# Kernel tuning notes

Hardware: AMD Instinct MI355X
Metric: run time of the kernel (lower is better)

## Reference

```python
import jax, jax.numpy as jnp
import numpy as np
import math

EMBED = 768
HEADS = 12
DK = EMBED // HEADS
FFN = 3072
NQ = 8
B, S = 4, 2048


def _layernorm(x, g, b, eps=1e-5):
    mu = jnp.mean(x, axis=-1, keepdims=True)
    var = jnp.var(x, axis=-1, keepdims=True)
    return (x - mu) * jax.lax.rsqrt(var + eps) * g + b


def setup_inputs() -> dict:
    key = jax.random.key(0)
    ks = jax.random.split(key, 16)
    std = 0.02
    inp = {
        "x": jax.random.normal(ks[0], (B, S, EMBED), dtype=jnp.float32),
        "mask": jnp.ones((B, S), dtype=jnp.int32),
        # attention projections (torch Linear: W [out, in])
        "wq": jax.random.normal(ks[1], (EMBED, EMBED), jnp.float32) * std,
        "bq": jnp.zeros((EMBED,), jnp.float32),
        "wk": jax.random.normal(ks[2], (EMBED, EMBED), jnp.float32) * std,
        "bk": jnp.zeros((EMBED,), jnp.float32),
        "wv": jax.random.normal(ks[3], (EMBED, EMBED), jnp.float32) * std,
        "bv": jnp.zeros((EMBED,), jnp.float32),
        "wo": jax.random.normal(ks[4], (EMBED, EMBED), jnp.float32) * std,
        "bo": jnp.zeros((EMBED,), jnp.float32),
        # layernorms
        "g1": jnp.ones((EMBED,), jnp.float32),
        "be1": jnp.zeros((EMBED,), jnp.float32),
        "g2": jnp.ones((EMBED,), jnp.float32),
        "be2": jnp.zeros((EMBED,), jnp.float32),
        # quantum FFN: trainable RY angles + two linears
        "theta": jax.random.normal(ks[5], (NQ,), jnp.float32) * 0.1,
        "w1": jax.random.normal(ks[6], (FFN, NQ), jnp.float32) * std,
        "b1": jnp.zeros((FFN,), jnp.float32),
        "w2": jax.random.normal(ks[7], (EMBED, FFN), jnp.float32) * std,
        "b2": jnp.zeros((EMBED,), jnp.float32),
    }
    return inp


def _block(x, mask, wq, bq, wk, bk, wv, bv, wo, bo, g1, be1, g2, be2,
           theta, w1, b1, w2, b2):
    b, s, _ = x.shape
    # --- multi-head attention (dropout = identity at eval) ---
    q = (x @ wq.T + bq).reshape(b, s, HEADS, DK)
    k = (x @ wk.T + bk).reshape(b, s, HEADS, DK)
    v = (x @ wv.T + bv).reshape(b, s, HEADS, DK)
    scores = jnp.einsum("bqhd,bkhd->bhqk", q, k) / math.sqrt(DK)
    scores = jnp.where(mask[:, None, None, :] == 0, -1e9, scores)
    attn = jax.nn.softmax(scores, axis=-1)
    ctx = jnp.einsum("bhqk,bkhd->bqhd", attn, v).reshape(b, s, EMBED)
    attn_out = ctx @ wo.T + bo
    x = _layernorm(x + attn_out, g1, be1)
    # --- quantum FFN: RY(x_i) then RY(theta_i) on |0>, <Z> = cos(x_i+theta_i)
    # (product state, no entanglement -> exact closed form, fully batched)
    meas = jnp.cos(x[..., :NQ] + theta)            # [b, s, NQ]
    h = jax.nn.relu(meas @ w1.T + b1)              # [b, s, FFN]
    ffn_out = h @ w2.T + b2                        # [b, s, EMBED]
    return _layernorm(x + ffn_out, g2, be2)


def reference(x, mask, wq, bq, wk, bk, wv, bv, wo, bo, g1, be1, g2, be2,
              theta, w1, b1, w2, b2):
    return _block(x, mask, wq, bq, wk, bk, wv, bv, wo, bo,
                  g1, be1, g2, be2, theta, w1, b1, w2, b2)
```

## Files before the change

kernel.cpp:

```cpp
#include <hip/hip_runtime.h>
#include <hip/hip_bf16.h>


typedef __bf16 bf16_t;
typedef bf16_t bf16x4 __attribute__((ext_vector_type(4)));
typedef bf16_t bf16x8 __attribute__((ext_vector_type(8)));
typedef float floatx4 __attribute__((ext_vector_type(4)));

#define LOG2E 1.44269504088896f

__device__ __forceinline__ void gload16(const bf16_t* g, bf16_t* l) {
    __builtin_amdgcn_global_load_lds(
        (const __attribute__((address_space(1))) unsigned int*)g,
        (__attribute__((address_space(3))) unsigned int*)l,
        16, 0, 0);
}

__device__ __forceinline__ int swz(int row, int col) {
    return row * 64 + (col ^ ((row & 7) << 3));
}

__global__ __launch_bounds__(256)
void prep(const float* __restrict__ x,
          const float* __restrict__ wq, const float* __restrict__ wk,
          const float* __restrict__ wv, const float* __restrict__ wo,
          const float* __restrict__ w2, const float* __restrict__ w1,
          const float* __restrict__ bq, const float* __restrict__ bk,
          const float* __restrict__ bv,
          bf16_t* __restrict__ xb, bf16_t* __restrict__ wqkv,
          bf16_t* __restrict__ wob, bf16_t* __restrict__ w2b,
          bf16_t* __restrict__ w1b, float* __restrict__ bqkv)
{
    const int seg = blockIdx.y;
    const int idx = blockIdx.x * 256 + threadIdx.x;
    if (seg == 0) {
        if (idx >= 1572864) return;
        const float4 f = ((const float4*)x)[idx];
        bf16x4 o = {(bf16_t)f.x, (bf16_t)f.y, (bf16_t)f.z, (bf16_t)f.w};
        ((bf16x4*)xb)[idx] = o;
    } else if (seg == 1) {
        if (idx >= 442368) return;
        const int e = idx * 4;
        float4 f = (e < 589824) ? ((const float4*)wq)[idx]
                 : (e < 1179648) ? ((const float4*)wk)[idx - 147456]
                                 : ((const float4*)wv)[idx - 294912];
        if (e < 589824) { f.x *= 0.125f; f.y *= 0.125f; f.z *= 0.125f; f.w *= 0.125f; }
        bf16x4 o = {(bf16_t)f.x, (bf16_t)f.y, (bf16_t)f.z, (bf16_t)f.w};
        ((bf16x4*)wqkv)[idx] = o;
    } else if (seg == 2) {
        if (idx >= 147456) return;
        const float4 f = ((const float4*)wo)[idx];
        bf16x4 o = {(bf16_t)f.x, (bf16_t)f.y, (bf16_t)f.z, (bf16_t)f.w};
        ((bf16x4*)wob)[idx] = o;
    } else if (seg == 3) {
        if (idx >= 589824) return;
        const float4 f = ((const float4*)w2)[idx];
        bf16x4 o = {(bf16_t)f.x, (bf16_t)f.y, (bf16_t)f.z, (bf16_t)f.w};
        ((bf16x4*)w2b)[idx] = o;
    } else if (seg == 4) {
        if (idx >= 576) return;
        const int e = idx * 4;
        float4 f = (e < 768) ? ((const float4*)bq)[idx]
                 : (e < 1536) ? ((const float4*)bk)[idx - 192]
                              : ((const float4*)bv)[idx - 384];
        if (e < 768) { f.x *= 0.125f; f.y *= 0.125f; f.z *= 0.125f; f.w *= 0.125f; }
        ((float4*)bqkv)[idx] = f;
    } else {
        if (idx >= 6144) return;
        const float4 f = ((const float4*)w1)[idx];
        bf16x4 o = {(bf16_t)f.x, (bf16_t)f.y, (bf16_t)f.z, (bf16_t)f.w};
        ((bf16x4*)w1b)[idx] = o;
    }
}

template<typename TC>
__global__ __launch_bounds__(256)
void gemm_bb(const bf16_t* __restrict__ A, const bf16_t* __restrict__ W,
             const float* __restrict__ bias, TC* __restrict__ C,
             int kPer, int lda, int ldw, int ldc, int splitStride)
{
    __shared__ __align__(16) bf16_t As[2][4096];
    __shared__ __align__(16) bf16_t Bs[2][4096];
    const int tid  = threadIdx.x;
    const int wave = tid >> 6;
    const int lane = tid & 63;
    const int wm = (wave >> 1) * 64;
    const int wn = (wave & 1) * 64;

    const int nwg  = gridDim.x * gridDim.y;
    const int flat = blockIdx.y * gridDim.x + blockIdx.x;
    const int swzb = (flat & 7) * (nwg >> 3) + (flat >> 3);
    const int bm = (swzb / gridDim.x) * 128;
    const int bn = (swzb % gridDim.x) * 128;

    const int fr = lane & 15;
    const int fk = (lane >> 4) * 8;

    const int kBeg = blockIdx.z * kPer;
    const int kEnd = kBeg + kPer;
    C += (size_t)blockIdx.z * splitStride;

    const int srow = tid >> 2;
    const int scol = (tid & 3) * 8;

    floatx4 acc[4][4] = {};

    const bf16_t* gA = A + (size_t)(bm + srow) * lda + scol;
    const bf16_t* gB = W + (size_t)(bn + srow) * ldw + scol;

#define STAGE(buf, kk)                                              \
    {   const bf16_t* ga = gA + (kk);                               \
        const bf16_t* gb = gB + (kk);                               \
        gload16(ga,                    &As[buf][tid * 8]);          \
        gload16(ga + (size_t)64 * lda, &As[buf][tid * 8 + 2048]);   \
        gload16(gb,                    &Bs[buf][tid * 8]);          \
        gload16(gb + (size_t)64 * ldw, &Bs[buf][tid * 8 + 2048]);   \
    }

    STAGE(0, kBeg);
    __syncthreads();

    int cur = 0;
    for (int k0 = kBeg; k0 < kEnd; k0 += 32) {
        if (k0 + 32 < kEnd) STAGE(cur ^ 1, k0 + 32);

        bf16x8 fa[4], fb[4];
        #pragma unroll
        for (int i = 0; i < 4; ++i) {
            fa[i] = *(const bf16x8*)&As[cur][(wm + i * 16 + fr) * 32 + fk];
            fb[i] = *(const bf16x8*)&Bs[cur][(wn + i * 16 + fr) * 32 + fk];
        }
        #pragma unroll
        for (int mi = 0; mi < 4; ++mi)
            #pragma unroll
            for (int ni = 0; ni < 4; ++ni)
                acc[mi][ni] = __builtin_amdgcn_mfma_f32_16x16x32_bf16(
                    fa[mi], fb[ni], acc[mi][ni], 0, 0, 0);

        __syncthreads();
        cur ^= 1;
    }
#undef STAGE

    const int fg = (lane >> 4) * 4;
    const bool addb = (blockIdx.z == 0);
    #pragma unroll
    for (int mi = 0; mi < 4; ++mi) {
        #pragma unroll
        for (int ni = 0; ni < 4; ++ni) {
            const int col = bn + wn + ni * 16 + fr;
            const float bv = addb ? bias[col] : 0.f;
            #pragma unroll
            for (int r = 0; r < 4; ++r) {
                const int row = bm + wm + mi * 16 + fg + r;
                C[(size_t)row * ldc + col] = (TC)(acc[mi][ni][r] + bv);
            }
        }
    }
}

__global__ __launch_bounds__(256)
void attn_mfma(const bf16_t* __restrict__ qkv, const int* __restrict__ mask,
               bf16_t* __restrict__ ctx)
{
    __shared__ __align__(16) bf16_t KsL[4096];
    __shared__ __align__(16) bf16_t VtL[4096];
    __shared__ __align__(16) bf16_t PlL[4][2048];
    __shared__ float mbL[64];

    const int flat = blockIdx.x;
    const int swzb = (flat & 7) * 96 + (flat >> 3);
    const int bh = swzb >> 4;
    const int b = bh / 12, h = bh % 12;
    const int tid  = threadIdx.x;
    const int wave = tid >> 6;
    const int lane = tid & 63;
    const int g    = lane >> 4;
    const int fr   = lane & 15;
    const int qbase = (swzb & 15) * 128 + wave * 32;

    bf16x8 qf[2][2];
    #pragma unroll
    for (int qt = 0; qt < 2; ++qt)
        #pragma unroll
        for (int s = 0; s < 2; ++s) {
            const size_t tok = (size_t)(b * 2048 + qbase + qt * 16 + fr);
            qf[qt][s] = *(const bf16x8*)(qkv + tok * 2304 + h * 64 + s * 32 + g * 8);
        }

    floatx4 o[2][4] = {};
    float lsum[2] = {0.f, 0.f};

    const int skey = tid & 63;
    const int sgrp = tid >> 6;

    bf16x8 rk0, rk1, rv0, rv1;
    float  rmb;
    {
        const size_t ktok = (size_t)(b * 2048 + skey) * 2304 + h * 64;
        rk0 = *(const bf16x8*)(qkv + ktok + 768 + sgrp * 16);
        rk1 = *(const bf16x8*)(qkv + ktok + 768 + sgrp * 16 + 8);
        rv0 = *(const bf16x8*)(qkv + ktok + 1536 + sgrp * 16);
        rv1 = *(const bf16x8*)(qkv + ktok + 1536 + sgrp * 16 + 8);
        rmb = (mask[b * 2048 + skey] == 0) ? -1e9f : 0.f;
    }

    for (int kt = 0; kt < 32; ++kt) {
        __syncthreads();
        *(bf16x8*)&KsL[swz(skey, sgrp * 16)]     = rk0;
        *(bf16x8*)&KsL[swz(skey, sgrp * 16 + 8)] = rk1;
        #pragma unroll
        for (int j = 0; j < 8; ++j) {
            VtL[swz(sgrp * 16 + j,     skey)] = rv0[j];
            VtL[swz(sgrp * 16 + 8 + j, skey)] = rv1[j];
        }
        if (tid < 64) mbL[tid] = rmb;
        __syncthreads();

        if (kt + 1 < 32) {
            const size_t ktok = (size_t)(b * 2048 + (kt + 1) * 64 + skey) * 2304 + h * 64;
            rk0 = *(const bf16x8*)(qkv + ktok + 768 + sgrp * 16);
            rk1 = *(const bf16x8*)(qkv + ktok + 768 + sgrp * 16 + 8);
            rv0 = *(const bf16x8*)(qkv + ktok + 1536 + sgrp * 16);
            rv1 = *(const bf16x8*)(qkv + ktok + 1536 + sgrp * 16 + 8);
            rmb = (mask[b * 2048 + (kt + 1) * 64 + skey] == 0) ? -1e9f : 0.f;
        }

        floatx4 st_[2][4] = {};
        #pragma unroll
        for (int s = 0; s < 2; ++s) {
            bf16x8 kf[4];
            #pragma unroll
            for (int ct = 0; ct < 4; ++ct)
                kf[ct] = *(const bf16x8*)&KsL[swz(ct * 16 + fr, s * 32 + g * 8)];
            #pragma unroll
            for (int qt = 0; qt < 2; ++qt)
                #pragma unroll
                for (int ct = 0; ct < 4; ++ct)
                    st_[qt][ct] = __builtin_amdgcn_mfma_f32_16x16x32_bf16(
                        kf[ct], qf[qt][s], st_[qt][ct], 0, 0, 0);
        }

        #pragma unroll
        for (int qt = 0; qt < 2; ++qt) {
            #pragma unroll
            for (int ct = 0; ct < 4; ++ct) {
                const float4 mb4 = *(const float4*)&mbL[ct * 16 + g * 4];
                const float mbr[4] = { mb4.x, mb4.y, mb4.z, mb4.w };
                bf16x4 pw;
                #pragma unroll
                for (int r = 0; r < 4; ++r) {
                    const float p = __builtin_amdgcn_exp2f(
                        fmaf(st_[qt][ct][r], LOG2E, mbr[r]));
                    lsum[qt] += p;
                    pw[r] = (bf16_t)p;
                }
                *(bf16x4*)&PlL[wave][swz(qt * 16 + fr, ct * 16 + g * 4)] = pw;
            }
        }

        #pragma unroll
        for (int st2 = 0; st2 < 2; ++st2) {
            bf16x8 pf[2];
            #pragma unroll
            for (int qt = 0; qt < 2; ++qt)
                pf[qt] = *(const bf16x8*)&PlL[wave][swz(qt * 16 + fr, st2 * 32 + g * 8)];
            #pragma unroll
            for (int dt = 0; dt < 4; ++dt) {
                const bf16x8 vf = *(const bf16x8*)&VtL[swz(dt * 16 + fr, st2 * 32 + g * 8)];
                #pragma unroll
                for (int qt = 0; qt < 2; ++qt)
                    o[qt][dt] = __builtin_amdgcn_mfma_f32_16x16x32_bf16(
                        pf[qt], vf, o[qt][dt], 0, 0, 0);
            }
        }
    }

    #pragma unroll
    for (int qt = 0; qt < 2; ++qt) {
        float lf = lsum[qt];
        lf += __shfl_xor(lf, 16, 64);
        lf += __shfl_xor(lf, 32, 64);
        float inv[4];
        #pragma unroll
        for (int r = 0; r < 4; ++r) {
            const float lv = __shfl(lf, (lane & 48) + g * 4 + r, 64);
            inv[r] = 1.f / lv;
        }
        #pragma unroll
        for (int dt = 0; dt < 4; ++dt)
            #pragma unroll
            for (int r = 0; r < 4; ++r) {
                const size_t row = (size_t)(b * 2048 + qbase + qt * 16 + g * 4 + r);
                ctx[row * 768 + h * 64 + dt * 16 + fr] = (bf16_t)(o[qt][dt][r] * inv[r]);
            }
    }
}

__global__ __launch_bounds__(256)
void ln_fuse(const float* __restrict__ xin, const float* __restrict__ proj,
             const float* __restrict__ proj2,
             const float* __restrict__ g, const float* __restrict__ be,
             float* __restrict__ out,
             const float* __restrict__ theta, float* __restrict__ meas)
{
    const int wave = threadIdx.x >> 6;
    const int lane = threadIdx.x & 63;
    const int row  = blockIdx.x * 4 + wave;
    const size_t base = (size_t)row * 768;

    float4 v[3];
    float s1 = 0.f, s2 = 0.f;
    #pragma unroll
    for (int i = 0; i < 3; ++i) {
        const int c4 = lane + i * 64;
        const float4 a  = ((const float4*)(xin  + base))[c4];
        const float4 p  = ((const float4*)(proj + base))[c4];
        const float4 p2 = ((const float4*)(proj2 + base))[c4];
        v[i].x = a.x + p.x + p2.x;
        v[i].y = a.y + p.y + p2.y;
        v[i].z = a.z + p.z + p2.z;
        v[i].w = a.w + p.w + p2.w;
        s1 += v[i].x + v[i].y + v[i].z + v[i].w;
        s2 += v[i].x*v[i].x + v[i].y*v[i].y + v[i].z*v[i].z + v[i].w*v[i].w;
    }
    #pragma unroll
    for (int mk = 32; mk >= 1; mk >>= 1) {
        s1 += __shfl_xor(s1, mk, 64);
        s2 += __shfl_xor(s2, mk, 64);
    }
    const float mu   = s1 * (1.f / 768.f);
    const float var  = s2 * (1.f / 768.f) - mu * mu;
    const float rinv = rsqrtf(var + 1e-5f);

    #pragma unroll
    for (int i = 0; i < 3; ++i) {
        const int c4 = lane + i * 64;
        const float4 gg = ((const float4*)g)[c4];
        const float4 bb = ((const float4*)be)[c4];
        float4 o;
        o.x = (v[i].x - mu) * rinv * gg.x + bb.x;
        o.y = (v[i].y - mu) * rinv * gg.y + bb.y;
        o.z = (v[i].z - mu) * rinv * gg.z + bb.z;
        o.w = (v[i].w - mu) * rinv * gg.w + bb.w;
        ((float4*)(out + base))[c4] = o;
        if (i == 0 && meas != nullptr && lane < 2) {
            meas[row * 8 + lane * 4 + 0] = cosf(o.x + theta[lane * 4 + 0]);
            meas[row * 8 + lane * 4 + 1] = cosf(o.y + theta[lane * 4 + 1]);
            meas[row * 8 + lane * 4 + 2] = cosf(o.z + theta[lane * 4 + 2]);
            meas[row * 8 + lane * 4 + 3] = cosf(o.w + theta[lane * 4 + 3]);
        }
    }
}

__global__ __launch_bounds__(256)
void ffn1(const float* __restrict__ meas, const bf16_t* __restrict__ w1b,
          const float* __restrict__ b1, bf16_t* __restrict__ h)
{
    const int row0 = blockIdx.x * 4;
    __shared__ float ms[4][8];
    if (threadIdx.x < 32)
        ms[threadIdx.x >> 3][threadIdx.x & 7] = meas[row0 * 8 + threadIdx.x];
    __syncthreads();
    #pragma unroll
    for (int i = 0; i < 12; ++i) {
        const int f = threadIdx.x + i * 256;
        const bf16x8 w = *(const bf16x8*)(w1b + f * 8);
        float wv[8];
        #pragma unroll
        for (int j = 0; j < 8; ++j) wv[j] = (float)w[j];
        const float bias = b1[f];
        #pragma unroll
        for (int r = 0; r < 4; ++r) {
            float v = bias;
            #pragma unroll
            for (int j = 0; j < 8; ++j) v += ms[r][j] * wv[j];
            h[(size_t)(row0 + r) * 3072 + f] = (bf16_t)fmaxf(v, 0.f);
        }
    }
}

extern "C" void kernel_launch(void* const* d_in, const int* in_sizes, int n_in,
                              void* d_out, int out_size, void* d_ws, size_t ws_size,
                              hipStream_t stream)
{
    const float* x     = (const float*)d_in[0];
    const int*   mask  = (const int*)d_in[1];
    const float* wq    = (const float*)d_in[2];
    const float* bq    = (const float*)d_in[3];
    const float* wk    = (const float*)d_in[4];
    const float* bk    = (const float*)d_in[5];
    const float* wv    = (const float*)d_in[6];
    const float* bv    = (const float*)d_in[7];
    const float* wo    = (const float*)d_in[8];
    const float* bo    = (const float*)d_in[9];
    const float* g1    = (const float*)d_in[10];
    const float* be1   = (const float*)d_in[11];
    const float* g2    = (const float*)d_in[12];
    const float* be2   = (const float*)d_in[13];
    const float* theta = (const float*)d_in[14];
    const float* w1    = (const float*)d_in[15];
    const float* b1    = (const float*)d_in[16];
    const float* w2    = (const float*)d_in[17];
    const float* b2    = (const float*)d_in[18];
    float* out = (float*)d_out;

    char* ws = (char*)d_ws;
    bf16_t* qkv    = (bf16_t*)(ws + 0);
    bf16_t* ctx    = (bf16_t*)(ws + 37748736);
    float*  attnp  = (float*)(ws + 50331648);
    float*  y      = (float*)(ws + 100663296);
    float*  meas   = (float*)(ws + 125829120);
    bf16_t* xb     = (bf16_t*)(ws + 126091264);
    bf16_t* wqkv   = (bf16_t*)(ws + 138674176);
    bf16_t* wob    = (bf16_t*)(ws + 142213120);
    bf16_t* w2b    = (bf16_t*)(ws + 143392768);
    float*  bqkv   = (float*)(ws + 148111360);
    bf16_t* w1b    = (bf16_t*)(ws + 148120576);
    float*  ffnp   = (float*)(ws + 0);
    bf16_t* h      = (bf16_t*)(ws + 50331648);

    const dim3 blk(256);

    prep<<<dim3(6144, 6), blk, 0, stream>>>(x, wq, wk, wv, wo, w2, w1, bq, bk, bv,
                                            xb, wqkv, wob, w2b, w1b, bqkv);

    gemm_bb<bf16_t><<<dim3(18, 64, 1), blk, 0, stream>>>(
        xb, wqkv, bqkv, qkv, 768, 768, 768, 2304, 0);

    attn_mfma<<<dim3(768), blk, 0, stream>>>(qkv, mask, ctx);

    gemm_bb<float><<<dim3(6, 64, 2), blk, 0, stream>>>(
        ctx, wob, bo, attnp, 384, 768, 768, 768, 6291456);

    ln_fuse<<<dim3(2048), blk, 0, stream>>>(x, attnp, attnp + 6291456,
                                            g1, be1, y, theta, meas);

    ffn1<<<dim3(2048), blk, 0, stream>>>(meas, w1b, b1, h);

    gemm_bb<float><<<dim3(6, 64, 2), blk, 0, stream>>>(
        h, w2b, b2, ffnp, 1536, 3072, 3072, 768, 6291456);

    ln_fuse<<<dim3(2048), blk, 0, stream>>>(y, ffnp, ffnp + 6291456,
                                            g2, be2, out, nullptr, nullptr);
}
```

Baseline: 292.0 us.

## Compute softmax row sums via extra ones-column MFMA and use padded LDS

Replaces the scalar per-lane accumulation of softmax denominators with an extra MFMA against a ones row appended to the transposed V tile, so the row sum comes out of the matrix unit. It also drops the XOR-swizzled LDS layout in favour of arrays padded to a row stride of 72 elements to avoid bank conflicts. The sum is now taken over the bf16-rounded probabilities, which changes numerics slightly, and it adds MFMA work plus extra LDS.

Result: faster. 279.1 us (-4.4%).

```diff
diff --git a/kernel.cpp b/kernel.cpp
--- a/kernel.cpp
+++ b/kernel.cpp
@@ -14,10 +14,6 @@
         (const __attribute__((address_space(1))) unsigned int*)g,
         (__attribute__((address_space(3))) unsigned int*)l,
         16, 0, 0);
-}
-
-__device__ __forceinline__ int swz(int row, int col) {
-    return row * 64 + (col ^ ((row & 7) << 3));
 }
 
 __global__ __launch_bounds__(256)
@@ -163,10 +159,10 @@
 void attn_mfma(const bf16_t* __restrict__ qkv, const int* __restrict__ mask,
                bf16_t* __restrict__ ctx)
 {
-    __shared__ __align__(16) bf16_t KsL[4096];
-    __shared__ __align__(16) bf16_t VtL[4096];
-    __shared__ __align__(16) bf16_t PlL[4][2048];
-    __shared__ float mbL[64];
+    __shared__ bf16_t Ks[64][72];
+    __shared__ bf16_t Vt[80][72];
+    __shared__ float  mb_s[64];
+    __shared__ bf16_t Pl[4][32][72];
 
     const int flat = blockIdx.x;
     const int swzb = (flat & 7) * 96 + (flat >> 3);
@@ -179,6 +175,11 @@
     const int fr   = lane & 15;
     const int qbase = (swzb & 15) * 128 + wave * 32;
 
+    for (int idx = tid; idx < 16 * 72; idx += 256) {
+        const int rr = idx / 72, cc = idx % 72;
+        Vt[64 + rr][cc] = (bf16_t)(rr == 0 ? 1.f : 0.f);
+    }
+
     bf16x8 qf[2][2];
     #pragma unroll
     for (int qt = 0; qt < 2; ++qt)
@@ -189,7 +190,7 @@
         }
 
     floatx4 o[2][4] = {};
-    float lsum[2] = {0.f, 0.f};
+    floatx4 oe[2] = {};
 
     const int skey = tid & 63;
     const int sgrp = tid >> 6;
@@ -207,14 +208,14 @@
 
     for (int kt = 0; kt < 32; ++kt) {
         __syncthreads();
-        *(bf16x8*)&KsL[swz(skey, sgrp * 16)]     = rk0;
-        *(bf16x8*)&KsL[swz(skey, sgrp * 16 + 8)] = rk1;
+        *(bf16x8*)&Ks[skey][sgrp * 16]     = rk0;
+        *(bf16x8*)&Ks[skey][sgrp * 16 + 8] = rk1;
         #pragma unroll
         for (int j = 0; j < 8; ++j) {
-            VtL[swz(sgrp * 16 + j,     skey)] = rv0[j];
-            VtL[swz(sgrp * 16 + 8 + j, skey)] = rv1[j];
-        }
-        if (tid < 64) mbL[tid] = rmb;
+            Vt[sgrp * 16 + j][skey]     = rv0[j];
+            Vt[sgrp * 16 + 8 + j][skey] = rv1[j];
+        }
+        if (tid < 64) mb_s[tid] = rmb;
         __syncthreads();
 
         if (kt + 1 < 32) {
@@ -232,7 +233,7 @@
             bf16x8 kf[4];
             #pragma unroll
             for (int ct = 0; ct < 4; ++ct)
-                kf[ct] = *(const bf16x8*)&KsL[swz(ct * 16 + fr, s * 32 + g * 8)];
+                kf[ct] = *(const bf16x8*)&Ks[ct * 16 + fr][s * 32 + g * 8];
             #pragma unroll
             for (int qt = 0; qt < 2; ++qt)
                 #pragma unroll
@@ -245,17 +246,14 @@
         for (int qt = 0; qt < 2; ++qt) {
             #pragma unroll
             for (int ct = 0; ct < 4; ++ct) {
-                const float4 mb4 = *(const float4*)&mbL[ct * 16 + g * 4];
+                const float4 mb4 = *(const float4*)&mb_s[ct * 16 + g * 4];
                 const float mbr[4] = { mb4.x, mb4.y, mb4.z, mb4.w };
                 bf16x4 pw;
                 #pragma unroll
-                for (int r = 0; r < 4; ++r) {
-                    const float p = __builtin_amdgcn_exp2f(
+                for (int r = 0; r < 4; ++r)
+                    pw[r] = (bf16_t)__builtin_amdgcn_exp2f(
                         fmaf(st_[qt][ct][r], LOG2E, mbr[r]));
-                    lsum[qt] += p;
-                    pw[r] = (bf16_t)p;
-                }
-                *(bf16x4*)&PlL[wave][swz(qt * 16 + fr, ct * 16 + g * 4)] = pw;
+                *(bf16x4*)&Pl[wave][qt * 16 + fr][ct * 16 + g * 4] = pw;
             }
         }
 
@@ -264,27 +262,29 @@
             bf16x8 pf[2];
             #pragma unroll
             for (int qt = 0; qt < 2; ++qt)
-                pf[qt] = *(const bf16x8*)&PlL[wave][swz(qt * 16 + fr, st2 * 32 + g * 8)];
+                pf[qt] = *(const bf16x8*)&Pl[wave][qt * 16 + fr][st2 * 32 + g * 8];
             #pragma unroll
             for (int dt = 0; dt < 4; ++dt) {
-                const bf16x8 vf = *(const bf16x8*)&VtL[swz(dt * 16 + fr, st2 * 32 + g * 8)];
+                const bf16x8 vf = *(const bf16x8*)&Vt[dt * 16 + fr][st2 * 32 + g * 8];
                 #pragma unroll
                 for (int qt = 0; qt < 2; ++qt)
                     o[qt][dt] = __builtin_amdgcn_mfma_f32_16x16x32_bf16(
                         pf[qt], vf, o[qt][dt], 0, 0, 0);
             }
+            const bf16x8 vo = *(const bf16x8*)&Vt[64 + fr][st2 * 32 + g * 8];
+            #pragma unroll
+            for (int qt = 0; qt < 2; ++qt)
+                oe[qt] = __builtin_amdgcn_mfma_f32_16x16x32_bf16(
+                    pf[qt], vo, oe[qt], 0, 0, 0);
         }
     }
 
     #pragma unroll
     for (int qt = 0; qt < 2; ++qt) {
-        float lf = lsum[qt];
-        lf += __shfl_xor(lf, 16, 64);
-        lf += __shfl_xor(lf, 32, 64);
         float inv[4];
         #pragma unroll
         for (int r = 0; r < 4; ++r) {
-            const float lv = __shfl(lf, (lane & 48) + g * 4 + r, 64);
+            const float lv = __shfl(oe[qt][r], (lane & 48), 64);
             inv[r] = 1.f / lv;
         }
         #pragma unroll
```
